# Optimization experiments

Hardware: AMD Instinct MI355X
Metric: run time of the kernel (lower is better)

Reference implementation:

```python
import jax, jax.numpy as jnp
import numpy as np

C = 32
KSHAPE = (C, C, 3, 3)  # (C_out, C_in, kH, kW)
BN_EPS = 1e-5


def _binary_act(x):
    # forward: sign(x); backward: identity clipped to |x|<1 (STE)
    xc = jnp.clip(x, -1.0, 1.0)
    return jax.lax.stop_gradient(jnp.sign(x) - xc) + xc


def _binarize_weight(w_flat, shape):
    w = w_flat.reshape(shape)
    scale = jax.lax.stop_gradient(jnp.mean(jnp.abs(w)))  # global scalar scale, detached
    wc = jnp.clip(w, -1.0, 1.0)
    # forward: scale*sign(w); backward flows through clamp(w,-1,1)
    return jax.lax.stop_gradient(scale * jnp.sign(w) - wc) + wc


def _bi_conv_bn(x, w_flat, gamma, beta, stride):
    xb = _binary_act(x)
    w = _binarize_weight(w_flat, KSHAPE)
    y = jax.lax.conv_general_dilated(
        xb, w, window_strides=(stride, stride), padding=[(1, 1), (1, 1)],
        dimension_numbers=('NCHW', 'OIHW', 'NCHW'))
    # BatchNorm2d in training mode (batch stats, biased variance)
    m = jnp.mean(y, axis=(0, 2, 3), keepdims=True)
    v = jnp.mean((y - m) ** 2, axis=(0, 2, 3), keepdims=True)
    yhat = (y - m) * jax.lax.rsqrt(v + BN_EPS)
    return gamma.reshape(1, -1, 1, 1) * yhat + beta.reshape(1, -1, 1, 1)


def setup_inputs() -> dict:
    key = jax.random.key(0)
    k1, k2, k3 = jax.random.split(key, 3)
    return {
        'x': jax.random.normal(k1, (32, C, 160, 160), dtype=jnp.float32),
        'w1': jax.random.normal(k2, (C * C * 9, 1), dtype=jnp.float32) * 0.05,
        'gamma1': jnp.ones((C,), dtype=jnp.float32),
        'beta1': jnp.zeros((C,), dtype=jnp.float32),
        'w2': jax.random.normal(k3, (C * C * 9, 1), dtype=jnp.float32) * 0.05,
        'gamma2': jnp.ones((C,), dtype=jnp.float32),
        'beta2': jnp.zeros((C,), dtype=jnp.float32),
    }


def reference(x, w1, gamma1, beta1, w2, gamma2, beta2):
    # bireal residual block, stride=1 => skip_op is Identity
    inner = _bi_conv_bn(x, w1, gamma1, beta1, 1) + x
    out = _bi_conv_bn(inner, w2, gamma2, beta2, 1) + inner
    return out
```

## Files before the change

kernel.cpp:

```cpp
#include <hip/hip_runtime.h>
#include <stdint.h>

#define NIMG 32
#define CH 32
#define HH 160
#define WW 160
#define HWL (HH*WW)
#define PRS 164
#define PHH 162
#define PIMG (PHH*PRS)
#define NPIX (NIMG*HWL)
#define HALO_WORDS 968

#define OFF_P     0
#define OFF_P2    3400704
#define OFF_INNER (OFF_P2 + 3400704)
#define OFF_WP    (OFF_INNER + 52428800)
#define OFF_CORR  (OFF_WP + 2304)
#define OFF_SC    (OFF_CORR + 2304)
#define OFF_SB    (OFF_SC + 128)

struct StatLine {
  int s1; int pad0; unsigned long long s2; char pad[112];
};

#define AS1 __attribute__((address_space(1)))
#define AS3 __attribute__((address_space(3)))
__device__ __forceinline__ void dma16(const float* g, float* l) {
  __builtin_amdgcn_global_load_lds((const AS1 void*)g, (AS3 void*)l, 16, 0, 0);
}

__device__ __forceinline__ unsigned short f2bf(float f) {
  unsigned u = __float_as_uint(f);
  u += 0x7fffu + ((u >> 16) & 1u);
  return (unsigned short)(u >> 16);
}
__device__ __forceinline__ float bf2f(unsigned short u) {
  return __uint_as_float((uint32_t)u << 16);
}

__device__ __forceinline__ void conv4(const uint32_t r[3][6], const uint32_t* wsh,
                                      int co, int& a0, int& a1, int& a2, int& a3)
{
  a0 = a1 = a2 = a3 = 0;
  #pragma unroll
  for (int dy = 0; dy < 3; ++dy) {
    #pragma unroll
    for (int dx = 0; dx < 3; ++dx) {
      uint32_t wvv = wsh[co * 9 + dy * 3 + dx];
      a0 += __popc(r[dy][0 + dx] ^ wvv);
      a1 += __popc(r[dy][1 + dx] ^ wvv);
      a2 += __popc(r[dy][2 + dx] ^ wvv);
      a3 += __popc(r[dy][3 + dx] ^ wvv);
    }
  }
}

__global__ __launch_bounds__(256) void pack_prep(const float* __restrict__ x,
    const float* __restrict__ w1, const float* __restrict__ w2,
    uint32_t* __restrict__ P, uint32_t* __restrict__ P2, uint32_t* __restrict__ WP,
    int* __restrict__ CORR, float* __restrict__ SC, StatLine* __restrict__ SB)
{
  __shared__ float lds[16384];
  const int tid = threadIdx.x;
  const int b = blockIdx.x;

  if (b >= 1600) {
    if (b == 1842) {
      int* z = (int*)SB;
      for (int i = tid; i < 2048; i += 256) z[i] = 0;
      float* wl  = lds;
      float* red = lds + 9216;
      uint32_t* wpl = (uint32_t*)(lds + 9600);
      for (int cv = 0; cv < 2; ++cv) {
        const float* w = cv ? w2 : w1;
        float s = 0.f;
        #pragma unroll
        for (int j = 0; j < 9; ++j) {
          float4 v = *reinterpret_cast<const float4*>(w + (j * 256 + tid) * 4);
          *reinterpret_cast<float4*>(wl + (j * 256 + tid) * 4) = v;
          s += fabsf(v.x) + fabsf(v.y) + fabsf(v.z) + fabsf(v.w);
        }
        red[tid] = s;
        __syncthreads();
        for (int st = 128; st > 0; st >>= 1) {
          if (tid < st) red[tid] += red[tid + st];
          __syncthreads();
        }
        if (tid == 0) SC[cv] = red[0] / 9216.0f;
        for (int i = tid; i < 288; i += 256) {
          int co = i / 9, t = i - co * 9;
          uint32_t bw = 0;
          for (int ci = 0; ci < 32; ++ci)
            bw |= (wl[(co * 32 + ci) * 9 + t] > 0.0f) ? (1u << ci) : 0u;
          WP[cv * 288 + i] = bw;
          wpl[i] = bw;
        }
        __syncthreads();
        for (int i = tid; i < 288; i += 256) {
          int cls = i / 32, co = i - cls * 32;
          int hc = cls / 3, wc = cls - hc * 3;
          int corr = 0;
          for (int t = 0; t < 9; ++t) {
            int dy = t / 3 - 1, dx = t % 3 - 1;
            bool inval = (hc == 0 && dy == -1) || (hc == 2 && dy == 1) ||
                         (wc == 0 && dx == -1) || (wc == 2 && dx == 1);
            if (inval) corr += 32 - 2 * __popc(wpl[co * 9 + t]);
          }
          CORR[cv * 288 + cls * 32 + co] = corr;
        }
        __syncthreads();
      }
    } else {
      int k = (b - 1600) * 256 + tid;
      uint32_t* buf = (k < 32 * HALO_WORDS) ? P : P2;
      int j = k % (32 * HALO_WORDS);
      int img = j / HALO_WORDS;
      int r = j - img * HALO_WORDS;
      int pr, pc;
      if (r < 164)      { pr = 0;   pc = r; }
      else if (r < 328) { pr = 161; pc = r - 164; }
      else {
        int k2 = r - 328;
        pr = 1 + (k2 >> 2);
        int q = k2 & 3;
        pc = (q == 0) ? 0 : (160 + q);
      }
      buf[img * PIMG + pr * PRS + pc] = 0;
    }
    return;
  }

  int n = b / 50;
  int p0 = (b - n * 50) * 512;
  const float* xb = x + (size_t)n * CH * HWL + p0;
  #pragma unroll
  for (int it = 0; it < 16; ++it) {
    int c = it * 2 + (tid >> 7);
    const float* g = xb + (size_t)c * HWL + (tid & 127) * 4;
    float* l = lds + it * 1024 + (tid >> 6) * 256;
    dma16(g, l);
  }
  __syncthreads();

  const float2* l2 = (const float2*)lds;
  uint32_t b0 = 0, b1 = 0;
  #pragma unroll
  for (int c = 0; c < 32; ++c) {
    float2 v = l2[c * 256 + tid];
    if (v.x > 0.f) b0 |= 1u << c;
    if (v.y > 0.f) b1 |= 1u << c;
  }
  int pxg = p0 + tid * 2;
  int h = pxg / WW, w = pxg - h * WW;
  uint32_t* pw = P + n * PIMG + (h + 1) * PRS + (w + 1);
  pw[0] = b0; pw[1] = b1;
}

__global__ __launch_bounds__(256) void conv_stats(const uint32_t* __restrict__ P,
    const uint32_t* __restrict__ WP, const int* __restrict__ CORR,
    StatLine* __restrict__ sb)
{
  __shared__ uint32_t wsh[288];
  __shared__ int csh[288];
  __shared__ int ls1[32], ls2[32];
  const int tid = threadIdx.x;
  for (int i = tid; i < 288; i += 256) { wsh[i] = WP[i]; csh[i] = CORR[i]; }
  if (tid < 32) { ls1[tid] = 0; ls2[tid] = 0; }
  __syncthreads();

  int g = blockIdx.x * 256 + tid;
  int w4 = g % 40;
  int t1 = g / 40;
  int h = t1 % 160;
  int n = t1 / 160;

  const uint32_t* base = P + n * PIMG + h * PRS + w4 * 4;
  uint32_t r[3][6];
  #pragma unroll
  for (int dy = 0; dy < 3; ++dy) {
    uint4 a = *reinterpret_cast<const uint4*>(base + dy * PRS);
    uint2 bw = *reinterpret_cast<const uint2*>(base + dy * PRS + 4);
    r[dy][0] = a.x; r[dy][1] = a.y; r[dy][2] = a.z; r[dy][3] = a.w;
    r[dy][4] = bw.x; r[dy][5] = bw.y;
  }

  int rowc = (h == 0) ? 0 : ((h == 159) ? 6 : 3);
  int cls0  = rowc + ((w4 == 0) ? 0 : 1);
  int cls12 = rowc + 1;
  int cls3  = rowc + ((w4 == 39) ? 2 : 1);
  int lane = tid & 63;

  #pragma unroll
  for (int co = 0; co < 32; ++co) {
    int a0, a1, a2, a3;
    conv4(r, wsh, co, a0, a1, a2, a3);
    int d0 = 288 - 2 * a0 - csh[cls0 * 32 + co];
    int d1 = 288 - 2 * a1 - csh[cls12 * 32 + co];
    int d2 = 288 - 2 * a2 - csh[cls12 * 32 + co];
    int d3 = 288 - 2 * a3 - csh[cls3 * 32 + co];
    int ds = d0 + d1 + d2 + d3;
    int sq = d0 * d0 + d1 * d1 + d2 * d2 + d3 * d3;
    #pragma unroll
    for (int off = 32; off > 0; off >>= 1) {
      ds += __shfl_down(ds, off);
      sq += __shfl_down(sq, off);
    }
    if (lane == 0) { atomicAdd(&ls1[co], ds); atomicAdd(&ls2[co], sq); }
  }
  __syncthreads();
  if (tid < 32) {
    atomicAdd(&sb[tid].s1, ls1[tid]);
    atomicAdd(&sb[tid].s2, (unsigned long long)(long long)ls2[tid]);
  }
}

__global__ __launch_bounds__(256, 2) void conv_bn1(const uint32_t* __restrict__ P,
    const uint32_t* __restrict__ WP, const int* __restrict__ CORR,
    const float* __restrict__ x, const float* __restrict__ SCp,
    const StatLine* __restrict__ sb, const float* __restrict__ gamma,
    const float* __restrict__ beta, unsigned short* __restrict__ INNER,
    uint32_t* __restrict__ P2)
{
  __shared__ uint32_t wsh[288];
  __shared__ int csh[288];
  __shared__ float Ash[32], Bsh[32];
  const int tid = threadIdx.x;
  for (int i = tid; i < 288; i += 256) { wsh[i] = WP[i]; csh[i] = CORR[i]; }
  if (tid < 32) {
    double sc = (double)SCp[0];
    double m  = sc * (double)sb[tid].s1 / (double)NPIX;
    double ms = sc * sc * (double)(long long)sb[tid].s2 / (double)NPIX;
    float inv = (float)(1.0 / sqrt(ms - m * m + 1e-5));
    float gm = gamma[tid];
    Ash[tid] = gm * inv * (float)sc;
    Bsh[tid] = beta[tid] - gm * inv * (float)m;
  }
  __syncthreads();

  int g = blockIdx.x * 256 + tid;
  int w4 = g % 40;
  int t1 = g / 40;
  int h = t1 % 160;
  int n = t1 / 160;

  const uint32_t* base = P + n * PIMG + h * PRS + w4 * 4;
  uint32_t r[3][6];
  #pragma unroll
  for (int dy = 0; dy < 3; ++dy) {
    uint4 a = *reinterpret_cast<const uint4*>(base + dy * PRS);
    uint2 bw = *reinterpret_cast<const uint2*>(base + dy * PRS + 4);
    r[dy][0] = a.x; r[dy][1] = a.y; r[dy][2] = a.z; r[dy][3] = a.w;
    r[dy][4] = bw.x; r[dy][5] = bw.y;
  }
  int rowc = (h == 0) ? 0 : ((h == 159) ? 6 : 3);
  int cls0  = rowc + ((w4 == 0) ? 0 : 1);
  int cls12 = rowc + 1;
  int cls3  = rowc + ((w4 == 39) ? 2 : 1);

  int i = h * WW + w4 * 4;
  size_t pbase = (size_t)n * CH * HWL + i;

  float4 xv[32];
  #pragma unroll
  for (int j = 0; j < 32; ++j)
    xv[j] = *reinterpret_cast<const float4*>(x + pbase + (size_t)j * HWL);

  uint32_t bb0 = 0, bb1 = 0, bb2 = 0, bb3 = 0;
  #pragma unroll
  for (int co = 0; co < 32; ++co) {
    int a0, a1, a2, a3;
    conv4(r, wsh, co, a0, a1, a2, a3);
    int d0 = 288 - 2 * a0 - csh[cls0 * 32 + co];
    int d1 = 288 - 2 * a1 - csh[cls12 * 32 + co];
    int d2 = 288 - 2 * a2 - csh[cls12 * 32 + co];
    int d3 = 288 - 2 * a3 - csh[cls3 * 32 + co];
    float A = Ash[co], Bv = Bsh[co];
    float v0 = fmaf(A, (float)d0, Bv) + xv[co].x;
    float v1 = fmaf(A, (float)d1, Bv) + xv[co].y;
    float v2 = fmaf(A, (float)d2, Bv) + xv[co].z;
    float v3 = fmaf(A, (float)d3, Bv) + xv[co].w;
    ushort4 o; o.x = f2bf(v0); o.y = f2bf(v1); o.z = f2bf(v2); o.w = f2bf(v3);
    *reinterpret_cast<ushort4*>(INNER + pbase + (size_t)co * HWL) = o;
    uint32_t m = 1u << co;
    if (v0 > 0.f) bb0 |= m;
    if (v1 > 0.f) bb1 |= m;
    if (v2 > 0.f) bb2 |= m;
    if (v3 > 0.f) bb3 |= m;
  }
  uint32_t* pw = P2 + n * PIMG + (h + 1) * PRS + (w4 * 4 + 1);
  pw[0] = bb0; pw[1] = bb1; pw[2] = bb2; pw[3] = bb3;
}

__global__ __launch_bounds__(256, 2) void conv_bn2(const uint32_t* __restrict__ P2,
    const uint32_t* __restrict__ WP, const int* __restrict__ CORR,
    const unsigned short* __restrict__ INNER, const float* __restrict__ SCp,
    const StatLine* __restrict__ sb, const float* __restrict__ gamma,
    const float* __restrict__ beta, float* __restrict__ out)
{
  __shared__ uint32_t wsh[288];
  __shared__ int csh[288];
  __shared__ float Ash[32], Bsh[32];
  const int tid = threadIdx.x;
  for (int i = tid; i < 288; i += 256) { wsh[i] = WP[i]; csh[i] = CORR[i]; }
  if (tid < 32) {
    double sc = (double)SCp[0];
    double m  = sc * (double)sb[tid].s1 / (double)NPIX;
    double ms = sc * sc * (double)(long long)sb[tid].s2 / (double)NPIX;
    float inv = (float)(1.0 / sqrt(ms - m * m + 1e-5));
    float gm = gamma[tid];
    Ash[tid] = gm * inv * (float)sc;
    Bsh[tid] = beta[tid] - gm * inv * (float)m;
  }
  __syncthreads();

  int g = blockIdx.x * 256 + tid;
  int w4 = g % 40;
  int t1 = g / 40;
  int h = t1 % 160;
  int n = t1 / 160;

  const uint32_t* base = P2 + n * PIMG + h * PRS + w4 * 4;
  uint32_t r[3][6];
  #pragma unroll
  for (int dy = 0; dy < 3; ++dy) {
    uint4 a = *reinterpret_cast<const uint4*>(base + dy * PRS);
    uint2 bw = *reinterpret_cast<const uint2*>(base + dy * PRS + 4);
    r[dy][0] = a.x; r[dy][1] = a.y; r[dy][2] = a.z; r[dy][3] = a.w;
    r[dy][4] = bw.x; r[dy][5] = bw.y;
  }
  int rowc = (h == 0) ? 0 : ((h == 159) ? 6 : 3);
  int cls0  = rowc + ((w4 == 0) ? 0 : 1);
  int cls12 = rowc + 1;
  int cls3  = rowc + ((w4 == 39) ? 2 : 1);

  int i = h * WW + w4 * 4;
  size_t pbase = (size_t)n * CH * HWL + i;

  ushort4 iv[32];
  #pragma unroll
  for (int j = 0; j < 32; ++j)
    iv[j] = *reinterpret_cast<const ushort4*>(INNER + pbase + (size_t)j * HWL);

  #pragma unroll
  for (int co = 0; co < 32; ++co) {
    int a0, a1, a2, a3;
    conv4(r, wsh, co, a0, a1, a2, a3);
    int d0 = 288 - 2 * a0 - csh[cls0 * 32 + co];
    int d1 = 288 - 2 * a1 - csh[cls12 * 32 + co];
    int d2 = 288 - 2 * a2 - csh[cls12 * 32 + co];
    int d3 = 288 - 2 * a3 - csh[cls3 * 32 + co];
    float A = Ash[co], Bv = Bsh[co];
    float4 o;
    o.x = fmaf(A, (float)d0, Bv) + bf2f(iv[co].x);
    o.y = fmaf(A, (float)d1, Bv) + bf2f(iv[co].y);
    o.z = fmaf(A, (float)d2, Bv) + bf2f(iv[co].z);
    o.w = fmaf(A, (float)d3, Bv) + bf2f(iv[co].w);
    *reinterpret_cast<float4*>(out + pbase + (size_t)co * HWL) = o;
  }
}

extern "C" void kernel_launch(void* const* d_in, const int* in_sizes, int n_in,
                              void* d_out, int out_size, void* d_ws, size_t ws_size,
                              hipStream_t stream)
{
  (void)in_sizes; (void)n_in; (void)out_size; (void)ws_size;
  const float* x  = (const float*)d_in[0];
  const float* w1 = (const float*)d_in[1];
  const float* g1 = (const float*)d_in[2];
  const float* b1 = (const float*)d_in[3];
  const float* w2 = (const float*)d_in[4];
  const float* g2 = (const float*)d_in[5];
  const float* b2 = (const float*)d_in[6];
  float* out = (float*)d_out;
  char* ws = (char*)d_ws;

  uint32_t*       P     = (uint32_t*)(ws + OFF_P);
  uint32_t*       P2    = (uint32_t*)(ws + OFF_P2);
  unsigned short* INNER = (unsigned short*)(ws + OFF_INNER);
  uint32_t*       WP    = (uint32_t*)(ws + OFF_WP);
  int*            CORR  = (int*)(ws + OFF_CORR);
  float*          SC    = (float*)(ws + OFF_SC);
  StatLine*       SB    = (StatLine*)(ws + OFF_SB);

  pack_prep<<<1843, 256, 0, stream>>>(x, w1, w2, P, P2, WP, CORR, SC, SB);
  conv_stats<<<800, 256, 0, stream>>>(P, WP, CORR, SB);
  conv_bn1<<<800, 256, 0, stream>>>(P, WP, CORR, x, SC, SB, g1, b1, INNER, P2);
  conv_stats<<<800, 256, 0, stream>>>(P2, WP + 288, CORR + 288, SB + 32);
  conv_bn2<<<800, 256, 0, stream>>>(P2, WP + 288, CORR + 288, INNER, SC + 1, SB + 32, g2, b2, out);
}
```

Before: 174.6 us.

## Stage residual inputs through LDS via async DMA in BN-apply kernels

Both BN-apply kernels now copy the residual operand (fp32 x in the first, bf16 inner in the second) for 30 of 32 channels into shared memory with global_load_lds DMA. The copies are issued up front so they overlap the weight, stats and bit-window setup, which replaces 32 per-thread float4/ushort4 register loads. conv_bn1 also drops to 2 pixels per thread with 1600 blocks, and both kernels lose the min-2-blocks occupancy hint. This cuts register pressure and exposed load latency, at the cost of a large LDS footprint (about 60 KB per block) that may limit resident blocks per CU.

```diff
diff --git a/kernel.cpp b/kernel.cpp
--- a/kernel.cpp
+++ b/kernel.cpp
@@ -26,7 +26,7 @@
 
 #define AS1 __attribute__((address_space(1)))
 #define AS3 __attribute__((address_space(3)))
-__device__ __forceinline__ void dma16(const float* g, float* l) {
+__device__ __forceinline__ void dma16(const void* g, void* l) {
   __builtin_amdgcn_global_load_lds((const AS1 void*)g, (AS3 void*)l, 16, 0, 0);
 }
 
@@ -215,17 +215,33 @@
   }
 }
 
-__global__ __launch_bounds__(256, 2) void conv_bn1(const uint32_t* __restrict__ P,
+__global__ __launch_bounds__(256) void conv_bn1(const uint32_t* __restrict__ P,
     const uint32_t* __restrict__ WP, const int* __restrict__ CORR,
     const float* __restrict__ x, const float* __restrict__ SCp,
     const StatLine* __restrict__ sb, const float* __restrict__ gamma,
     const float* __restrict__ beta, unsigned short* __restrict__ INNER,
     uint32_t* __restrict__ P2)
 {
+  __shared__ float xs[30 * 512];
   __shared__ uint32_t wsh[288];
   __shared__ int csh[288];
   __shared__ float Ash[32], Bsh[32];
   const int tid = threadIdx.x;
+  const int b = blockIdx.x;
+  int n = b / 50;
+  int p0 = (b - n * 50) * 512;
+  const float* xb = x + (size_t)n * CH * HWL + p0;
+
+  #pragma unroll
+  for (int it = 0; it < 15; ++it) {
+    int q = it * 4 + (tid >> 6);
+    const float* g = xb + (size_t)(q >> 1) * HWL + (q & 1) * 256 + (tid & 63) * 4;
+    dma16(g, xs + q * 256);
+  }
+  int px = p0 + tid * 2;
+  float2 x30 = *reinterpret_cast<const float2*>(xb + (size_t)30 * HWL + tid * 2);
+  float2 x31 = *reinterpret_cast<const float2*>(xb + (size_t)31 * HWL + tid * 2);
+
   for (int i = tid; i < 288; i += 256) { wsh[i] = WP[i]; csh[i] = CORR[i]; }
   if (tid < 32) {
     double sc = (double)SCp[0];
@@ -236,72 +252,81 @@
     Ash[tid] = gm * inv * (float)sc;
     Bsh[tid] = beta[tid] - gm * inv * (float)m;
   }
+
+  int h = px / WW;
+  int wloc = px - h * WW;
+  const uint32_t* base = P + n * PIMG + h * PRS + wloc;
+  uint32_t r2[3][4];
+  #pragma unroll
+  for (int dy = 0; dy < 3; ++dy) {
+    uint2 u0 = *reinterpret_cast<const uint2*>(base + dy * PRS);
+    uint2 u1 = *reinterpret_cast<const uint2*>(base + dy * PRS + 2);
+    r2[dy][0] = u0.x; r2[dy][1] = u0.y; r2[dy][2] = u1.x; r2[dy][3] = u1.y;
+  }
+  int rowc = (h == 0) ? 0 : ((h == 159) ? 6 : 3);
+  int cls0 = rowc + ((wloc == 0) ? 0 : 1);
+  int cls1 = rowc + ((wloc == 158) ? 2 : 1);
+
   __syncthreads();
 
-  int g = blockIdx.x * 256 + tid;
-  int w4 = g % 40;
-  int t1 = g / 40;
-  int h = t1 % 160;
-  int n = t1 / 160;
-
-  const uint32_t* base = P + n * PIMG + h * PRS + w4 * 4;
-  uint32_t r[3][6];
-  #pragma unroll
-  for (int dy = 0; dy < 3; ++dy) {
-    uint4 a = *reinterpret_cast<const uint4*>(base + dy * PRS);
-    uint2 bw = *reinterpret_cast<const uint2*>(base + dy * PRS + 4);
-    r[dy][0] = a.x; r[dy][1] = a.y; r[dy][2] = a.z; r[dy][3] = a.w;
-    r[dy][4] = bw.x; r[dy][5] = bw.y;
-  }
-  int rowc = (h == 0) ? 0 : ((h == 159) ? 6 : 3);
-  int cls0  = rowc + ((w4 == 0) ? 0 : 1);
-  int cls12 = rowc + 1;
-  int cls3  = rowc + ((w4 == 39) ? 2 : 1);
-
-  int i = h * WW + w4 * 4;
-  size_t pbase = (size_t)n * CH * HWL + i;
-
-  float4 xv[32];
-  #pragma unroll
-  for (int j = 0; j < 32; ++j)
-    xv[j] = *reinterpret_cast<const float4*>(x + pbase + (size_t)j * HWL);
-
-  uint32_t bb0 = 0, bb1 = 0, bb2 = 0, bb3 = 0;
+  size_t pbase = (size_t)n * CH * HWL + px;
+  uint32_t bb0 = 0, bb1 = 0;
   #pragma unroll
   for (int co = 0; co < 32; ++co) {
-    int a0, a1, a2, a3;
-    conv4(r, wsh, co, a0, a1, a2, a3);
+    int a0 = 0, a1 = 0;
+    #pragma unroll
+    for (int dy = 0; dy < 3; ++dy) {
+      #pragma unroll
+      for (int dx = 0; dx < 3; ++dx) {
+        uint32_t wvv = wsh[co * 9 + dy * 3 + dx];
+        a0 += __popc(r2[dy][dx] ^ wvv);
+        a1 += __popc(r2[dy][dx + 1] ^ wvv);
+      }
+    }
     int d0 = 288 - 2 * a0 - csh[cls0 * 32 + co];
-    int d1 = 288 - 2 * a1 - csh[cls12 * 32 + co];
-    int d2 = 288 - 2 * a2 - csh[cls12 * 32 + co];
-    int d3 = 288 - 2 * a3 - csh[cls3 * 32 + co];
+    int d1 = 288 - 2 * a1 - csh[cls1 * 32 + co];
+    float2 xv;
+    if (co < 30) xv = *reinterpret_cast<const float2*>(xs + co * 512 + tid * 2);
+    else         xv = (co == 30) ? x30 : x31;
     float A = Ash[co], Bv = Bsh[co];
-    float v0 = fmaf(A, (float)d0, Bv) + xv[co].x;
-    float v1 = fmaf(A, (float)d1, Bv) + xv[co].y;
-    float v2 = fmaf(A, (float)d2, Bv) + xv[co].z;
-    float v3 = fmaf(A, (float)d3, Bv) + xv[co].w;
-    ushort4 o; o.x = f2bf(v0); o.y = f2bf(v1); o.z = f2bf(v2); o.w = f2bf(v3);
-    *reinterpret_cast<ushort4*>(INNER + pbase + (size_t)co * HWL) = o;
+    float v0 = fmaf(A, (float)d0, Bv) + xv.x;
+    float v1 = fmaf(A, (float)d1, Bv) + xv.y;
+    ushort2 o; o.x = f2bf(v0); o.y = f2bf(v1);
+    *reinterpret_cast<ushort2*>(INNER + pbase + (size_t)co * HWL) = o;
     uint32_t m = 1u << co;
     if (v0 > 0.f) bb0 |= m;
     if (v1 > 0.f) bb1 |= m;
-    if (v2 > 0.f) bb2 |= m;
-    if (v3 > 0.f) bb3 |= m;
-  }
-  uint32_t* pw = P2 + n * PIMG + (h + 1) * PRS + (w4 * 4 + 1);
-  pw[0] = bb0; pw[1] = bb1; pw[2] = bb2; pw[3] = bb3;
-}
-
-__global__ __launch_bounds__(256, 2) void conv_bn2(const uint32_t* __restrict__ P2,
+  }
+  uint32_t* pw = P2 + n * PIMG + (h + 1) * PRS + (wloc + 1);
+  pw[0] = bb0; pw[1] = bb1;
+}
+
+__global__ __launch_bounds__(256) void conv_bn2(const uint32_t* __restrict__ P2,
     const uint32_t* __restrict__ WP, const int* __restrict__ CORR,
     const unsigned short* __restrict__ INNER, const float* __restrict__ SCp,
     const StatLine* __restrict__ sb, const float* __restrict__ gamma,
     const float* __restrict__ beta, float* __restrict__ out)
 {
+  __shared__ unsigned short is[30 * 1024];
   __shared__ uint32_t wsh[288];
   __shared__ int csh[288];
   __shared__ float Ash[32], Bsh[32];
   const int tid = threadIdx.x;
+  const int b = blockIdx.x;
+  int n = b / 25;
+  int p0 = (b - n * 25) * 1024;
+  const unsigned short* ib = INNER + (size_t)n * CH * HWL + p0;
+
+  #pragma unroll
+  for (int it = 0; it < 15; ++it) {
+    int q = it * 4 + (tid >> 6);
+    const unsigned short* g = ib + (size_t)(q >> 1) * HWL + (q & 1) * 512 + (tid & 63) * 8;
+    dma16(g, is + q * 512);
+  }
+  int px = p0 + tid * 4;
+  ushort4 i30 = *reinterpret_cast<const ushort4*>(ib + (size_t)30 * HWL + tid * 4);
+  ushort4 i31 = *reinterpret_cast<const ushort4*>(ib + (size_t)31 * HWL + tid * 4);
+
   for (int i = tid; i < 288; i += 256) { wsh[i] = WP[i]; csh[i] = CORR[i]; }
   if (tid < 32) {
     double sc = (double)SCp[0];
@@ -312,15 +337,10 @@
     Ash[tid] = gm * inv * (float)sc;
     Bsh[tid] = beta[tid] - gm * inv * (float)m;
   }
-  __syncthreads();
-
-  int g = blockIdx.x * 256 + tid;
-  int w4 = g % 40;
-  int t1 = g / 40;
-  int h = t1 % 160;
-  int n = t1 / 160;
-
-  const uint32_t* base = P2 + n * PIMG + h * PRS + w4 * 4;
+
+  int h = px / WW;
+  int wloc = px - h * WW;
+  const uint32_t* base = P2 + n * PIMG + h * PRS + wloc;
   uint32_t r[3][6];
   #pragma unroll
   for (int dy = 0; dy < 3; ++dy) {
@@ -330,18 +350,13 @@
     r[dy][4] = bw.x; r[dy][5] = bw.y;
   }
   int rowc = (h == 0) ? 0 : ((h == 159) ? 6 : 3);
-  int cls0  = rowc + ((w4 == 0) ? 0 : 1);
+  int cls0  = rowc + ((wloc == 0) ? 0 : 1);
   int cls12 = rowc + 1;
-  int cls3  = rowc + ((w4 == 39) ? 2 : 1);
-
-  int i = h * WW + w4 * 4;
-  size_t pbase = (size_t)n * CH * HWL + i;
-
-  ushort4 iv[32];
-  #pragma unroll
-  for (int j = 0; j < 32; ++j)
-    iv[j] = *reinterpret_cast<const ushort4*>(INNER + pbase + (size_t)j * HWL);
-
+  int cls3  = rowc + ((wloc == 156) ? 2 : 1);
+
+  __syncthreads();
+
+  size_t pbase = (size_t)n * CH * HWL + px;
   #pragma unroll
   for (int co = 0; co < 32; ++co) {
     int a0, a1, a2, a3;
@@ -350,12 +365,15 @@
     int d1 = 288 - 2 * a1 - csh[cls12 * 32 + co];
     int d2 = 288 - 2 * a2 - csh[cls12 * 32 + co];
     int d3 = 288 - 2 * a3 - csh[cls3 * 32 + co];
+    ushort4 iv;
+    if (co < 30) iv = *reinterpret_cast<const ushort4*>(is + co * 1024 + tid * 4);
+    else         iv = (co == 30) ? i30 : i31;
     float A = Ash[co], Bv = Bsh[co];
     float4 o;
-    o.x = fmaf(A, (float)d0, Bv) + bf2f(iv[co].x);
-    o.y = fmaf(A, (float)d1, Bv) + bf2f(iv[co].y);
-    o.z = fmaf(A, (float)d2, Bv) + bf2f(iv[co].z);
-    o.w = fmaf(A, (float)d3, Bv) + bf2f(iv[co].w);
+    o.x = fmaf(A, (float)d0, Bv) + bf2f(iv.x);
+    o.y = fmaf(A, (float)d1, Bv) + bf2f(iv.y);
+    o.z = fmaf(A, (float)d2, Bv) + bf2f(iv.z);
+    o.w = fmaf(A, (float)d3, Bv) + bf2f(iv.w);
     *reinterpret_cast<float4*>(out + pbase + (size_t)co * HWL) = o;
   }
 }
@@ -385,7 +403,7 @@
 
   pack_prep<<<1843, 256, 0, stream>>>(x, w1, w2, P, P2, WP, CORR, SC, SB);
   conv_stats<<<800, 256, 0, stream>>>(P, WP, CORR, SB);
-  conv_bn1<<<800, 256, 0, stream>>>(P, WP, CORR, x, SC, SB, g1, b1, INNER, P2);
+  conv_bn1<<<1600, 256, 0, stream>>>(P, WP, CORR, x, SC, SB, g1, b1, INNER, P2);
   conv_stats<<<800, 256, 0, stream>>>(P2, WP + 288, CORR + 288, SB + 32);
   conv_bn2<<<800, 256, 0, stream>>>(P2, WP + 288, CORR + 288, INNER, SC + 1, SB + 32, g2, b2, out);
 }
```

New measurement: 189.0 us. 8.3% more time.
